# Kernel tuning notes

Measured on AMD Instinct MI355X. Metric: run time of the kernel, lower is better.

## Reference

```python
import jax, jax.numpy as jnp
import numpy as np

N_NODES = 100000
N_EDGES = 1600000
D_IN = 128
D_H = 128
N_LAYERS = 3
N_OUT = 10
N_GRAPHS = 64


def setup_inputs() -> dict:
    key = jax.random.key(0)
    ks = jax.random.split(key, 12)
    glorot = lambda k, fi, fo: jax.random.normal(k, (fi, fo), jnp.float32) * np.sqrt(2.0 / (fi + fo))
    return {
        "x": jax.random.normal(ks[0], (N_NODES, D_IN), jnp.float32),
        "edge_index": jax.random.randint(ks[1], (2, N_EDGES), 0, N_NODES, jnp.int64 if jax.config.jax_enable_x64 else jnp.int32),
        "batch": jnp.sort(jax.random.randint(ks[2], (N_NODES,), 0, N_GRAPHS)),
        "target_size": N_GRAPHS,
        "W1": glorot(ks[3], D_IN, D_H), "b1": jnp.zeros((D_H,), jnp.float32),
        "W2": glorot(ks[4], D_H, D_H), "b2": jnp.zeros((D_H,), jnp.float32),
        "W3": glorot(ks[5], D_H, D_H), "b3": jnp.zeros((D_H,), jnp.float32),
        "lin1_w": glorot(ks[6], N_LAYERS * D_H, D_H), "lin1_b": jnp.zeros((D_H,), jnp.float32),
        "lin2_w": glorot(ks[7], D_H, N_OUT), "lin2_b": jnp.zeros((N_OUT,), jnp.float32),
    }


def _gcn_conv(x, src, dst, norm, W, b, n_nodes):
    # PyG GCNConv: h = X W; out[dst] += norm * h[src]; out += b
    h = x @ W
    msg = h[src] * norm[:, None]            # [E+N, D_H] gathered messages
    out = jax.ops.segment_sum(msg, dst, num_segments=n_nodes)
    return out + b


def reference(x, edge_index, batch, target_size, W1, b1, W2, b2, W3, b3,
              lin1_w, lin1_b, lin2_w, lin2_b):
    n = x.shape[0]
    loops = jnp.arange(n, dtype=edge_index.dtype)
    src = jnp.concatenate([edge_index[0], loops])   # add self-loops (PyG default)
    dst = jnp.concatenate([edge_index[1], loops])
    deg = jax.ops.segment_sum(jnp.ones_like(src, dtype=x.dtype), dst, num_segments=n)
    dinv = jnp.where(deg > 0, jax.lax.rsqrt(deg), 0.0)
    norm = dinv[src] * dinv[dst]                    # symmetric normalization

    h1 = jax.nn.relu(_gcn_conv(x, src, dst, norm, W1, b1, n))
    h2 = jax.nn.relu(_gcn_conv(h1, src, dst, norm, W2, b2, n))
    h3 = jax.nn.relu(_gcn_conv(h2, src, dst, norm, W3, b3, n))
    h = jnp.concatenate([h1, h2, h3], axis=-1)      # JumpingKnowledge 'cat' -> [N, 3*D_H]

    # global_mean_pool over graphs
    counts = jax.ops.segment_sum(jnp.ones((n,), x.dtype), batch, num_segments=target_size)
    pooled = jax.ops.segment_sum(h, batch, num_segments=target_size)
    pooled = pooled / jnp.maximum(counts, 1.0)[:, None]

    g = jax.nn.relu(pooled @ lin1_w + lin1_b)       # dropout is identity at inference
    logits = g @ lin2_w + lin2_b
    return jax.nn.log_softmax(logits, axis=-1)
```

## Files before the change

### kernel.cpp

```cpp
#include <hip/hip_runtime.h>

#define NN 100000
#define NE 1600000
#define DH 128
#define NG 64

#define NBUCKU 98
#define EPB 4096
#define NBLK_BIN 391
#define CAP 20480

#define LDH 136
#define LDF 132

typedef __attribute__((ext_vector_type(2))) _Float16 half2v;
typedef __attribute__((ext_vector_type(4))) _Float16 half4;
typedef __attribute__((ext_vector_type(8))) _Float16 half8;
typedef __attribute__((ext_vector_type(4))) float f32x4;

__device__ inline unsigned int enc8(_Float16 h) {
  unsigned short b = __builtin_bit_cast(unsigned short, h);
  unsigned short r = (unsigned short)(b + 0x7F + ((b >> 8) & 1));
  return (unsigned int)(r >> 8);
}
__device__ inline half2v d02(unsigned int u) {
  return __builtin_bit_cast(half2v, (u << 8) & 0xFF00FF00u);
}
__device__ inline half2v d13(unsigned int u) {
  return __builtin_bit_cast(half2v, u & 0xFF00FF00u);
}

#define DEC4(u)                                                                         \
  acc[0] += d02(u.x); acc[1] += d13(u.x); acc[2] += d02(u.y); acc[3] += d13(u.y);       \
  acc[4] += d02(u.z); acc[5] += d13(u.z); acc[6] += d02(u.w); acc[7] += d13(u.w);

__device__ inline void gather_rows(const unsigned char* __restrict__ bp,
                                   const int* __restrict__ csr_src,
                                   int p, int e, half2v (&acc)[8]) {
  if (p + 3 < e) {
    int j0 = csr_src[p], j1 = csr_src[p + 1], j2 = csr_src[p + 2], j3 = csr_src[p + 3];
    uint4 c0 = *(const uint4*)(bp + (size_t)j0 * DH);
    uint4 c1 = *(const uint4*)(bp + (size_t)j1 * DH);
    uint4 c2 = *(const uint4*)(bp + (size_t)j2 * DH);
    uint4 c3 = *(const uint4*)(bp + (size_t)j3 * DH);
    p += 4;
    int pb = (p + 3 < e) ? p : p - 4;
    j0 = csr_src[pb]; j1 = csr_src[pb + 1]; j2 = csr_src[pb + 2]; j3 = csr_src[pb + 3];
    while (p + 3 < e) {
      uint4 n0 = *(const uint4*)(bp + (size_t)j0 * DH);
      uint4 n1 = *(const uint4*)(bp + (size_t)j1 * DH);
      uint4 n2 = *(const uint4*)(bp + (size_t)j2 * DH);
      uint4 n3 = *(const uint4*)(bp + (size_t)j3 * DH);
      p += 4;
      int pb2 = (p + 3 < e) ? p : p - 4;
      j0 = csr_src[pb2]; j1 = csr_src[pb2 + 1]; j2 = csr_src[pb2 + 2]; j3 = csr_src[pb2 + 3];
      DEC4(c0); DEC4(c1); DEC4(c2); DEC4(c3);
      c0 = n0; c1 = n1; c2 = n2; c3 = n3;
    }
    DEC4(c0); DEC4(c1); DEC4(c2); DEC4(c3);
  }
  for (; p < e; ++p) {
    uint4 u0 = *(const uint4*)(bp + (size_t)csr_src[p] * DH);
    DEC4(u0);
  }
}


__global__ __launch_bounds__(256) void k_pre(const float* __restrict__ W0,
                                             const float* __restrict__ W1,
                                             const float* __restrict__ W2,
                                             _Float16* __restrict__ Wt) {
  __shared__ _Float16 tile[128][LDH];
  int l = blockIdx.x, t = threadIdx.x;
  const float* W = (l == 0) ? W0 : (l == 1) ? W1 : W2;
#pragma unroll
  for (int i = 0; i < 64; ++i) {
    int idx = i * 256 + t;
    int r = idx >> 7, c = idx & 127;
    tile[c][r] = (_Float16)W[r * DH + c];
  }
  __syncthreads();
#pragma unroll
  for (int i = 0; i < 8; ++i) {
    int idx = i * 256 + t;
    int n = idx >> 4, c = (idx & 15) * 8;
    *(half8*)&Wt[(size_t)l * DH * DH + n * DH + c] = *(const half8*)&tile[n][c];
  }
}


__global__ __launch_bounds__(256) void k_build(const int* __restrict__ esrc,
                                               const int* __restrict__ edst,
                                               const int* __restrict__ batch,
                                               int* __restrict__ bucketCursor,
                                               unsigned int* __restrict__ pairs,
                                               int* __restrict__ startg) {
  int b = blockIdx.x, t = threadIdx.x;
  int gtid = b * 256 + t;

  if (gtid < NN) {
    int bat = batch[gtid];
    int prev = (gtid == 0) ? -1 : batch[gtid - 1];
    for (int g = prev + 1; g <= bat; ++g) startg[g] = gtid;
    if (gtid == NN - 1)
      for (int g = bat + 1; g <= NG; ++g) startg[g] = NN;
  }

  __shared__ int h[NBUCKU];
  __shared__ int cur[NBUCKU];
  if (t < NBUCKU) h[t] = 0;
  __syncthreads();
  int base = b * EPB;
  int dv[EPB / 256];
#pragma unroll
  for (int i = 0; i < EPB / 256; ++i) {
    int e = base + i * 256 + t;
    dv[i] = (e < NE) ? edst[e] : -1;
    if (e < NE) atomicAdd(&h[dv[i] >> 10], 1);
  }
  __syncthreads();
  if (t < NBUCKU) {
    int rel = atomicAdd(&bucketCursor[t], h[t]);
    cur[t] = t * CAP + rel;
  }
  __syncthreads();
#pragma unroll
  for (int i = 0; i < EPB / 256; ++i) {
    int e = base + i * 256 + t;
    if (e < NE) {
      int d = dv[i];
      int q = atomicAdd(&cur[d >> 10], 1);
      pairs[q] = ((unsigned int)esrc[e] << 10) | (unsigned int)(d & 1023);
    }
  }
}


__global__ __launch_bounds__(256) void k_finalize(const unsigned int* __restrict__ pairs,
                                                  const int* __restrict__ bucketCursor,
                                                  int* __restrict__ offA,
                                                  int* __restrict__ offB,
                                                  float* __restrict__ dinv,
                                                  int* __restrict__ csr_src) {
  __shared__ int cnt[1024];
  __shared__ int tsum[256];
  int b = blockIdx.x, t = threadIdx.x;
  int nodeBase = b << 10;
  for (int i = t; i < 1024; i += 256) cnt[i] = 0;
  __syncthreads();
  int pStart = b * CAP;
  int pEnd = pStart + bucketCursor[b];
  for (int p = pStart + t; p < pEnd; p += 256)
    atomicAdd(&cnt[pairs[p] & 1023], 1);
  __syncthreads();
  int c0 = cnt[t * 4], c1 = cnt[t * 4 + 1], c2 = cnt[t * 4 + 2], c3 = cnt[t * 4 + 3];
  tsum[t] = c0 + c1 + c2 + c3;
  __syncthreads();
  for (int off = 1; off < 256; off <<= 1) {
    int v = (t >= off) ? tsum[t - off] : 0;
    __syncthreads();
    tsum[t] += v;
    __syncthreads();
  }
  int basep = pStart + ((t > 0) ? tsum[t - 1] : 0);
  int e0 = basep, e1 = basep + c0, e2 = e1 + c1, e3 = e2 + c2;
  __syncthreads();
  cnt[t * 4] = e0; cnt[t * 4 + 1] = e1; cnt[t * 4 + 2] = e2; cnt[t * 4 + 3] = e3;
  int g = nodeBase + t * 4;
  if (g < NN)     { offA[g] = e0;     offB[g] = e1;      dinv[g] = rsqrtf((float)c0 + 1.f); }
  if (g + 1 < NN) { offA[g + 1] = e1; offB[g + 1] = e2;  dinv[g + 1] = rsqrtf((float)c1 + 1.f); }
  if (g + 2 < NN) { offA[g + 2] = e2; offB[g + 2] = e3;  dinv[g + 2] = rsqrtf((float)c2 + 1.f); }
  if (g + 3 < NN) { offA[g + 3] = e3; offB[g + 3] = e3 + c3; dinv[g + 3] = rsqrtf((float)c3 + 1.f); }
  __syncthreads();
  for (int p = pStart + t; p < pEnd; p += 256) {
    unsigned int pr = pairs[p];
    int pos = atomicAdd(&cnt[pr & 1023], 1);
    csr_src[pos] = (int)(pr >> 10);
  }
}


template <bool F32IN>
__global__ __launch_bounds__(256) void k_gemm(const void* __restrict__ Ap,
                                              const _Float16* __restrict__ Wt,
                                              const float* __restrict__ dinv,
                                              unsigned char* __restrict__ Out8) {
  __shared__ _Float16 Wl[128 * LDH];
  int tid = threadIdx.x;
  int rowBase = blockIdx.x * 128;

#pragma unroll
  for (int i = 0; i < 8; ++i) {
    int chunk = tid + i * 256;
    int r = chunk >> 4, c = (chunk & 15) * 8;
    *(half8*)&Wl[r * LDH + c] = *(const half8*)(Wt + r * DH + c);
  }

  int wv = tid >> 6;
  int lane = tid & 63;
  int n16 = lane & 15;
  int quad = lane >> 4;

  int r0 = rowBase + wv * 32 + n16;
  int r1 = r0 + 16;

  half8 af[2][4];
  if (F32IN) {
    const float* A = (const float*)Ap;
#pragma unroll
    for (int kk = 0; kk < 4; ++kk) {
      half8 z = {};
      if (r0 < NN) {
        float4 lo = *(const float4*)(A + (size_t)r0 * DH + quad * 8 + kk * 32);
        float4 hi = *(const float4*)(A + (size_t)r0 * DH + quad * 8 + kk * 32 + 4);
        z = (half8){(_Float16)lo.x, (_Float16)lo.y, (_Float16)lo.z, (_Float16)lo.w,
                    (_Float16)hi.x, (_Float16)hi.y, (_Float16)hi.z, (_Float16)hi.w};
      }
      af[0][kk] = z;
      half8 z1 = {};
      if (r1 < NN) {
        float4 lo = *(const float4*)(A + (size_t)r1 * DH + quad * 8 + kk * 32);
        float4 hi = *(const float4*)(A + (size_t)r1 * DH + quad * 8 + kk * 32 + 4);
        z1 = (half8){(_Float16)lo.x, (_Float16)lo.y, (_Float16)lo.z, (_Float16)lo.w,
                     (_Float16)hi.x, (_Float16)hi.y, (_Float16)hi.z, (_Float16)hi.w};
      }
      af[1][kk] = z1;
    }
  } else {
    const _Float16* A = (const _Float16*)Ap;
#pragma unroll
    for (int kk = 0; kk < 4; ++kk) {
      half8 z = {};
      if (r0 < NN) z = *(const half8*)(A + (size_t)r0 * DH + quad * 8 + kk * 32);
      af[0][kk] = z;
      half8 z1 = {};
      if (r1 < NN) z1 = *(const half8*)(A + (size_t)r1 * DH + quad * 8 + kk * 32);
      af[1][kk] = z1;
    }
  }
  __syncthreads();

  f32x4 acc[2][8];
#pragma unroll
  for (int mt = 0; mt < 2; ++mt)
#pragma unroll
    for (int ct = 0; ct < 8; ++ct) acc[mt][ct] = (f32x4){0.f, 0.f, 0.f, 0.f};

  const _Float16* bp = &Wl[n16 * LDH + quad * 8];
#pragma unroll
  for (int kk = 0; kk < 4; ++kk) {
#pragma unroll
    for (int ct = 0; ct < 8; ++ct) {
      half8 bf = *(const half8*)(bp + (size_t)ct * 16 * LDH + kk * 32);
      acc[0][ct] = __builtin_amdgcn_mfma_f32_16x16x32_f16(af[0][kk], bf, acc[0][ct], 0, 0, 0);
      acc[1][ct] = __builtin_amdgcn_mfma_f32_16x16x32_f16(af[1][kk], bf, acc[1][ct], 0, 0, 0);
    }
  }

  float dv[2][4];
#pragma unroll
  for (int mt = 0; mt < 2; ++mt)
#pragma unroll
    for (int r = 0; r < 4; ++r) {
      int gr = rowBase + wv * 32 + mt * 16 + quad * 4 + r;
      dv[mt][r] = (gr < NN) ? dinv[gr] : 0.f;
    }

  __syncthreads();
#pragma unroll
  for (int mt = 0; mt < 2; ++mt)
#pragma unroll
    for (int ct = 0; ct < 8; ++ct)
#pragma unroll
      for (int r = 0; r < 4; ++r)
        Wl[(wv * 32 + mt * 16 + quad * 4 + r) * LDH + ct * 16 + n16] =
            (_Float16)(acc[mt][ct][r] * dv[mt][r]);
  __syncthreads();

#pragma unroll
  for (int i = 0; i < 8; ++i) {
    int chunk = tid + i * 256;
    int r = chunk >> 4, c = (chunk & 15) * 8;
    int gr = rowBase + r;
    if (gr < NN) {
      half8 v = *(const half8*)&Wl[r * LDH + c];
      unsigned int lo = enc8(v[0]) | (enc8(v[1]) << 8) | (enc8(v[2]) << 16) | (enc8(v[3]) << 24);
      unsigned int hi = enc8(v[4]) | (enc8(v[5]) << 8) | (enc8(v[6]) << 16) | (enc8(v[7]) << 24);
      uint2 st = {lo, hi};
      *(uint2*)(Out8 + (size_t)gr * DH + c) = st;
    }
  }
}


__global__ __launch_bounds__(512) void k_fused(const unsigned char* __restrict__ hs8_in,
                                               const int* __restrict__ csr_src,
                                               const int* __restrict__ offA,
                                               const int* __restrict__ offB,
                                               const float* __restrict__ dinv,
                                               const float* __restrict__ bias,
                                               const int* __restrict__ batch,
                                               const int* __restrict__ startg,
                                               float* __restrict__ pooled,
                                               int colOff,
                                               const _Float16* __restrict__ Wt,
                                               unsigned char* __restrict__ hs8_out) {
  __shared__ _Float16 Hl[64 * LDH];
  __shared__ _Float16 Wl[128 * LDH];
  int tid = threadIdx.x;
  int n0 = blockIdx.x * 64;

#pragma unroll
  for (int i = 0; i < 4; ++i) {
    int chunk = tid + i * 512;
    int r = chunk >> 4, c = (chunk & 15) * 8;
    *(half8*)&Wl[r * LDH + c] = *(const half8*)(Wt + r * DH + c);
  }

  int nd = tid >> 3;
  int part = tid & 7;
  int n = n0 + nd;
  bool valid = (n < NN);

  half2v acc[8];
#pragma unroll
  for (int i = 0; i < 8; ++i) acc[i] = (half2v){(_Float16)0, (_Float16)0};

  if (valid) {
    const unsigned char* bp = hs8_in + part * 16;
    uint4 us = *(const uint4*)(bp + (size_t)n * DH);
    DEC4(us);
    gather_rows(bp, csr_src, offA[n], offB[n], acc);
  }

  float dv = valid ? dinv[n] : 0.f;
#pragma unroll
  for (int w = 0; w < 4; ++w) {
    int dim = part * 16 + w * 4;
    float4 b4 = *(const float4*)(bias + dim);
    float h0 = valid ? fmaxf(fmaf((float)acc[2 * w][0], dv, b4.x), 0.f) : 0.f;
    float h1 = valid ? fmaxf(fmaf((float)acc[2 * w + 1][0], dv, b4.y), 0.f) : 0.f;
    float h2 = valid ? fmaxf(fmaf((float)acc[2 * w][1], dv, b4.z), 0.f) : 0.f;
    float h3 = valid ? fmaxf(fmaf((float)acc[2 * w + 1][1], dv, b4.w), 0.f) : 0.f;
    half4 hh = {(_Float16)h0, (_Float16)h1, (_Float16)h2, (_Float16)h3};
    *(half4*)&Hl[nd * LDH + dim] = hh;
  }
  __syncthreads();

  if (tid < DH) {
    int nEnd = (n0 + 64 < NN) ? n0 + 64 : NN;
    int gF = batch[n0];
    int gL = batch[nEnd - 1];
    for (int g = gF; g <= gL; ++g) {
      int rs = (startg[g] > n0) ? startg[g] : n0;
      int re = (startg[g + 1] < nEnd) ? startg[g + 1] : nEnd;
      if (re > rs) {
        float sum = 0.f;
        for (int r2 = rs; r2 < re; ++r2) sum += (float)Hl[(r2 - n0) * LDH + tid];
        atomicAdd(&pooled[g * (3 * DH) + colOff + tid], sum);
      }
    }
  }

  int wv = tid >> 6;
  int lane = tid & 63;
  int n16 = lane & 15;
  int quad = lane >> 4;
  int m16 = wv >> 1;
  int ctB = (wv & 1) * 4;

  f32x4 acc2[4];
#pragma unroll
  for (int ct = 0; ct < 4; ++ct) acc2[ct] = (f32x4){0.f, 0.f, 0.f, 0.f};

  const _Float16* ap = &Hl[(m16 * 16 + n16) * LDH + quad * 8];
#pragma unroll
  for (int kk = 0; kk < 4; ++kk) {
    half8 af = *(const half8*)(ap + kk * 32);
#pragma unroll
    for (int ct = 0; ct < 4; ++ct) {
      half8 bf = *(const half8*)&Wl[((ctB + ct) * 16 + n16) * LDH + quad * 8 + kk * 32];
      acc2[ct] = __builtin_amdgcn_mfma_f32_16x16x32_f16(af, bf, acc2[ct], 0, 0, 0);
    }
  }

  float dvo[4];
#pragma unroll
  for (int rr = 0; rr < 4; ++rr) {
    int gr = n0 + m16 * 16 + quad * 4 + rr;
    dvo[rr] = (gr < NN) ? dinv[gr] : 0.f;
  }

  __syncthreads();
#pragma unroll
  for (int ct = 0; ct < 4; ++ct)
#pragma unroll
    for (int rr = 0; rr < 4; ++rr)
      Hl[(m16 * 16 + quad * 4 + rr) * LDH + (ctB + ct) * 16 + n16] =
          (_Float16)(acc2[ct][rr] * dvo[rr]);
  __syncthreads();

#pragma unroll
  for (int i = 0; i < 2; ++i) {
    int chunk = tid + i * 512;
    int r = chunk >> 4, c = (chunk & 15) * 8;
    int gr = n0 + r;
    if (gr < NN) {
      half8 v = *(const half8*)&Hl[r * LDH + c];
      unsigned int lo = enc8(v[0]) | (enc8(v[1]) << 8) | (enc8(v[2]) << 16) | (enc8(v[3]) << 24);
      unsigned int hi = enc8(v[4]) | (enc8(v[5]) << 8) | (enc8(v[6]) << 16) | (enc8(v[7]) << 24);
      uint2 st = {lo, hi};
      *(uint2*)(hs8_out + (size_t)gr * DH + c) = st;
    }
  }
}


__global__ __launch_bounds__(512) void k_aggregate(const unsigned char* __restrict__ hs8,
                                                   const int* __restrict__ csr_src,
                                                   const int* __restrict__ offA,
                                                   const int* __restrict__ offB,
                                                   const float* __restrict__ dinv,
                                                   const float* __restrict__ bias,
                                                   const int* __restrict__ batch,
                                                   const int* __restrict__ startg,
                                                   float* __restrict__ pooled,
                                                   int colOff) {
  __shared__ float stage[64][LDF];
  int tid = threadIdx.x;
  int n0 = blockIdx.x * 64;
  int nd = tid >> 3;
  int part = tid & 7;
  int n = n0 + nd;
  bool valid = (n < NN);

  half2v acc[8];
#pragma unroll
  for (int i = 0; i < 8; ++i) acc[i] = (half2v){(_Float16)0, (_Float16)0};

  if (valid) {
    const unsigned char* bp = hs8 + part * 16;
    uint4 us = *(const uint4*)(bp + (size_t)n * DH);
    DEC4(us);
    gather_rows(bp, csr_src, offA[n], offB[n], acc);
  }

  float dv = valid ? dinv[n] : 0.f;
#pragma unroll
  for (int w = 0; w < 4; ++w) {
    int dim = part * 16 + w * 4;
    float4 b4 = *(const float4*)(bias + dim);
    float4 r;
    r.x = valid ? fmaxf(fmaf((float)acc[2 * w][0], dv, b4.x), 0.f) : 0.f;
    r.y = valid ? fmaxf(fmaf((float)acc[2 * w + 1][0], dv, b4.y), 0.f) : 0.f;
    r.z = valid ? fmaxf(fmaf((float)acc[2 * w][1], dv, b4.z), 0.f) : 0.f;
    r.w = valid ? fmaxf(fmaf((float)acc[2 * w + 1][1], dv, b4.w), 0.f) : 0.f;
    *(float4*)&stage[nd][dim] = r;
  }
  __syncthreads();

  if (tid < DH) {
    int nEnd = (n0 + 64 < NN) ? n0 + 64 : NN;
    int gF = batch[n0];
    int gL = batch[nEnd - 1];
    for (int g = gF; g <= gL; ++g) {
      int rs = (startg[g] > n0) ? startg[g] : n0;
      int re = (startg[g + 1] < nEnd) ? startg[g + 1] : nEnd;
      if (re > rs) {
        float sum = 0.f;
        for (int r2 = rs; r2 < re; ++r2) sum += stage[r2 - n0][tid];
        atomicAdd(&pooled[g * (3 * DH) + colOff + tid], sum);
      }
    }
  }
}


__global__ __launch_bounds__(128) void k_head(const float* __restrict__ pooled,
                                              const int* __restrict__ startg,
                                              const float* __restrict__ l1w,
                                              const float* __restrict__ l1b,
                                              const float* __restrict__ l2w,
                                              const float* __restrict__ l2b,
                                              float* __restrict__ out) {
  __shared__ float pr[3 * DH];
  __shared__ float grow[DH];
  __shared__ float lg[16];
  int g = blockIdx.x, t = threadIdx.x;
  float cnt = (float)(startg[g + 1] - startg[g]);
  float inv = 1.0f / fmaxf(cnt, 1.0f);
  for (int k = t; k < 3 * DH; k += 128) pr[k] = pooled[g * (3 * DH) + k] * inv;
  __syncthreads();
  float acc = l1b[t];
  for (int k = 0; k < 3 * DH; ++k) acc = fmaf(pr[k], l1w[k * DH + t], acc);
  grow[t] = fmaxf(acc, 0.f);
  __syncthreads();
  if (t < 10) {
    float a = l2b[t];
    for (int k = 0; k < DH; ++k) a = fmaf(grow[k], l2w[k * 10 + t], a);
    lg[t] = a;
  }
  __syncthreads();
  if (t < 10) {
    float m = lg[0];
    for (int i = 1; i < 10; ++i) m = fmaxf(m, lg[i]);
    float sum = 0.f;
    for (int i = 0; i < 10; ++i) sum += expf(lg[i] - m);
    out[g * 10 + t] = lg[t] - m - logf(sum);
  }
}


extern "C" void kernel_launch(void* const* d_in, const int* in_sizes, int n_in,
                              void* d_out, int out_size, void* d_ws, size_t ws_size,
                              hipStream_t stream) {
  const float* x = (const float*)d_in[0];
  const int* ei = (const int*)d_in[1];
  const int* esrc = ei;
  const int* edst = ei + NE;
  const int* batch = (const int*)d_in[2];
  const float* W0 = (const float*)d_in[4];
  const float* W1 = (const float*)d_in[6];
  const float* W2 = (const float*)d_in[8];
  const float* B[3] = {(const float*)d_in[5], (const float*)d_in[7], (const float*)d_in[9]};
  const float* l1w = (const float*)d_in[10];
  const float* l1b = (const float*)d_in[11];
  const float* l2w = (const float*)d_in[12];
  const float* l2b = (const float*)d_in[13];
  float* out = (float*)d_out;

  char* ws = (char*)d_ws;
  size_t off = 0;
  auto alloc = [&](size_t bytes) {
    char* p = ws + off;
    off = (off + bytes + 255) & ~(size_t)255;
    return p;
  };
  float* pooled = (float*)alloc((size_t)NG * 3 * DH * 4);
  int* bucketCursor = (int*)alloc(NBUCKU * 4);
  size_t msBytes = (size_t)NG * 3 * DH * 4 + 512;

  int* offA = (int*)alloc((size_t)NN * 4);
  int* offB = (int*)alloc((size_t)NN * 4);
  float* dinv = (float*)alloc((size_t)NN * 4);
  int* startg = (int*)alloc((NG + 1) * 4);
  _Float16* Wt = (_Float16*)alloc((size_t)3 * DH * DH * 2);
  unsigned char* hs8A = (unsigned char*)alloc((size_t)NN * DH);
  unsigned char* hs8B = (unsigned char*)alloc((size_t)NN * DH);
  unsigned int* pairs = (unsigned int*)alloc((size_t)NBUCKU * CAP * 4);
  int* csr_src = (int*)alloc((size_t)NBUCKU * CAP * 4);

  hipMemsetAsync(pooled, 0, msBytes, stream);

  k_pre<<<3, 256, 0, stream>>>(W0, W1, W2, Wt);
  k_build<<<NBLK_BIN, 256, 0, stream>>>(esrc, edst, batch, bucketCursor, pairs, startg);
  k_finalize<<<NBUCKU, 256, 0, stream>>>(pairs, bucketCursor, offA, offB, dinv, csr_src);

  k_gemm<true><<<(NN + 127) / 128, 256, 0, stream>>>((const void*)x, Wt, dinv, hs8A);

  int nFusedBlk = (NN + 63) / 64;
  k_fused<<<nFusedBlk, 512, 0, stream>>>(hs8A, csr_src, offA, offB, dinv, B[0], batch,
                                         startg, pooled, 0,
                                         Wt + (size_t)1 * DH * DH, hs8B);
  k_fused<<<nFusedBlk, 512, 0, stream>>>(hs8B, csr_src, offA, offB, dinv, B[1], batch,
                                         startg, pooled, DH,
                                         Wt + (size_t)2 * DH * DH, hs8A);

  k_aggregate<<<nFusedBlk, 512, 0, stream>>>(hs8A, csr_src, offA, offB, dinv, B[2],
                                             batch, startg, pooled, 2 * DH);

  k_head<<<NG, 128, 0, stream>>>(pooled, startg, l1w, l1b, l2w, l2b, out);
}
```

Measured before the change: 342.0 us.

## Use finer 256-node CSR buckets and fold weight transpose into build kernel

Buckets now cover 256 destination nodes instead of 1024, so the finalize kernel runs 391 blocks instead of 98 and each thread handles one node, with a smaller per-bucket capacity. The weight transpose/convert kernel is merged into the edge-binning kernel, where the first three blocks also write the transposed fp16 weights. This removes one launch and spreads the CSR build across more blocks. The cost is more global bucket atomics and more shared-memory use in k_build, plus a tighter 5120-entry capacity per bucket that could overflow on skewed degree distributions.

```diff
diff --git a/kernel.cpp b/kernel.cpp
--- a/kernel.cpp
+++ b/kernel.cpp
@@ -5,10 +5,10 @@
 #define DH 128
 #define NG 64
 
-#define NBUCKU 98
+#define NBUCK 391
 #define EPB 4096
 #define NBLK_BIN 391
-#define CAP 20480
+#define CAP 5120
 
 #define LDH 136
 #define LDF 132
@@ -66,37 +66,38 @@
 }
 
 
-__global__ __launch_bounds__(256) void k_pre(const float* __restrict__ W0,
-                                             const float* __restrict__ W1,
-                                             const float* __restrict__ W2,
-                                             _Float16* __restrict__ Wt) {
-  __shared__ _Float16 tile[128][LDH];
-  int l = blockIdx.x, t = threadIdx.x;
-  const float* W = (l == 0) ? W0 : (l == 1) ? W1 : W2;
-#pragma unroll
-  for (int i = 0; i < 64; ++i) {
-    int idx = i * 256 + t;
-    int r = idx >> 7, c = idx & 127;
-    tile[c][r] = (_Float16)W[r * DH + c];
-  }
-  __syncthreads();
-#pragma unroll
-  for (int i = 0; i < 8; ++i) {
-    int idx = i * 256 + t;
-    int n = idx >> 4, c = (idx & 15) * 8;
-    *(half8*)&Wt[(size_t)l * DH * DH + n * DH + c] = *(const half8*)&tile[n][c];
-  }
-}
-
-
 __global__ __launch_bounds__(256) void k_build(const int* __restrict__ esrc,
                                                const int* __restrict__ edst,
                                                const int* __restrict__ batch,
+                                               const float* __restrict__ W0,
+                                               const float* __restrict__ W1,
+                                               const float* __restrict__ W2,
                                                int* __restrict__ bucketCursor,
                                                unsigned int* __restrict__ pairs,
-                                               int* __restrict__ startg) {
+                                               int* __restrict__ startg,
+                                               _Float16* __restrict__ Wt) {
+  __shared__ _Float16 tile[128][LDH];
+  __shared__ int h[NBUCK];
+  __shared__ int cur[NBUCK];
   int b = blockIdx.x, t = threadIdx.x;
   int gtid = b * 256 + t;
+
+  if (b < 3) {
+    const float* W = (b == 0) ? W0 : (b == 1) ? W1 : W2;
+#pragma unroll
+    for (int i = 0; i < 64; ++i) {
+      int idx = i * 256 + t;
+      int r = idx >> 7, c = idx & 127;
+      tile[c][r] = (_Float16)W[r * DH + c];
+    }
+    __syncthreads();
+#pragma unroll
+    for (int i = 0; i < 8; ++i) {
+      int idx = i * 256 + t;
+      int n = idx >> 4, c = (idx & 15) * 8;
+      *(half8*)&Wt[(size_t)b * DH * DH + n * DH + c] = *(const half8*)&tile[n][c];
+    }
+  }
 
   if (gtid < NN) {
     int bat = batch[gtid];
@@ -106,9 +107,7 @@
       for (int g = bat + 1; g <= NG; ++g) startg[g] = NN;
   }
 
-  __shared__ int h[NBUCKU];
-  __shared__ int cur[NBUCKU];
-  if (t < NBUCKU) h[t] = 0;
+  for (int i = t; i < NBUCK; i += 256) h[i] = 0;
   __syncthreads();
   int base = b * EPB;
   int dv[EPB / 256];
@@ -116,12 +115,12 @@
   for (int i = 0; i < EPB / 256; ++i) {
     int e = base + i * 256 + t;
     dv[i] = (e < NE) ? edst[e] : -1;
-    if (e < NE) atomicAdd(&h[dv[i] >> 10], 1);
-  }
-  __syncthreads();
-  if (t < NBUCKU) {
-    int rel = atomicAdd(&bucketCursor[t], h[t]);
-    cur[t] = t * CAP + rel;
+    if (e < NE) atomicAdd(&h[dv[i] >> 8], 1);
+  }
+  __syncthreads();
+  for (int i = t; i < NBUCK; i += 256) {
+    int rel = atomicAdd(&bucketCursor[i], h[i]);
+    cur[i] = i * CAP + rel;
   }
   __syncthreads();
 #pragma unroll
@@ -129,8 +128,8 @@
     int e = base + i * 256 + t;
     if (e < NE) {
       int d = dv[i];
-      int q = atomicAdd(&cur[d >> 10], 1);
-      pairs[q] = ((unsigned int)esrc[e] << 10) | (unsigned int)(d & 1023);
+      int q = atomicAdd(&cur[d >> 8], 1);
+      pairs[q] = ((unsigned int)esrc[e] << 8) | (unsigned int)(d & 255);
     }
   }
 }
@@ -142,19 +141,19 @@
                                                   int* __restrict__ offB,
                                                   float* __restrict__ dinv,
                                                   int* __restrict__ csr_src) {
-  __shared__ int cnt[1024];
+  __shared__ int cnt[256];
   __shared__ int tsum[256];
   int b = blockIdx.x, t = threadIdx.x;
-  int nodeBase = b << 10;
-  for (int i = t; i < 1024; i += 256) cnt[i] = 0;
+  int g = (b << 8) + t;
+  cnt[t] = 0;
   __syncthreads();
   int pStart = b * CAP;
   int pEnd = pStart + bucketCursor[b];
   for (int p = pStart + t; p < pEnd; p += 256)
-    atomicAdd(&cnt[pairs[p] & 1023], 1);
-  __syncthreads();
-  int c0 = cnt[t * 4], c1 = cnt[t * 4 + 1], c2 = cnt[t * 4 + 2], c3 = cnt[t * 4 + 3];
-  tsum[t] = c0 + c1 + c2 + c3;
+    atomicAdd(&cnt[pairs[p] & 255], 1);
+  __syncthreads();
+  int c = cnt[t];
+  tsum[t] = c;
   __syncthreads();
   for (int off = 1; off < 256; off <<= 1) {
     int v = (t >= off) ? tsum[t - off] : 0;
@@ -163,19 +162,17 @@
     __syncthreads();
   }
   int basep = pStart + ((t > 0) ? tsum[t - 1] : 0);
-  int e0 = basep, e1 = basep + c0, e2 = e1 + c1, e3 = e2 + c2;
-  __syncthreads();
-  cnt[t * 4] = e0; cnt[t * 4 + 1] = e1; cnt[t * 4 + 2] = e2; cnt[t * 4 + 3] = e3;
-  int g = nodeBase + t * 4;
-  if (g < NN)     { offA[g] = e0;     offB[g] = e1;      dinv[g] = rsqrtf((float)c0 + 1.f); }
-  if (g + 1 < NN) { offA[g + 1] = e1; offB[g + 1] = e2;  dinv[g + 1] = rsqrtf((float)c1 + 1.f); }
-  if (g + 2 < NN) { offA[g + 2] = e2; offB[g + 2] = e3;  dinv[g + 2] = rsqrtf((float)c2 + 1.f); }
-  if (g + 3 < NN) { offA[g + 3] = e3; offB[g + 3] = e3 + c3; dinv[g + 3] = rsqrtf((float)c3 + 1.f); }
+  if (g < NN) {
+    offA[g] = basep;
+    offB[g] = basep + c;
+    dinv[g] = rsqrtf((float)c + 1.f);
+  }
+  cnt[t] = basep;
   __syncthreads();
   for (int p = pStart + t; p < pEnd; p += 256) {
     unsigned int pr = pairs[p];
-    int pos = atomicAdd(&cnt[pr & 1023], 1);
-    csr_src[pos] = (int)(pr >> 10);
+    int pos = atomicAdd(&cnt[pr & 255], 1);
+    csr_src[pos] = (int)(pr >> 8);
   }
 }
 
@@ -537,8 +534,8 @@
     return p;
   };
   float* pooled = (float*)alloc((size_t)NG * 3 * DH * 4);
-  int* bucketCursor = (int*)alloc(NBUCKU * 4);
-  size_t msBytes = (size_t)NG * 3 * DH * 4 + 512;
+  int* bucketCursor = (int*)alloc(NBUCK * 4);
+  size_t msBytes = ((size_t)NG * 3 * DH * 4 + NBUCK * 4 + 255) & ~(size_t)255;
 
   int* offA = (int*)alloc((size_t)NN * 4);
   int* offB = (int*)alloc((size_t)NN * 4);
@@ -547,14 +544,14 @@
   _Float16* Wt = (_Float16*)alloc((size_t)3 * DH * DH * 2);
   unsigned char* hs8A = (unsigned char*)alloc((size_t)NN * DH);
   unsigned char* hs8B = (unsigned char*)alloc((size_t)NN * DH);
-  unsigned int* pairs = (unsigned int*)alloc((size_t)NBUCKU * CAP * 4);
-  int* csr_src = (int*)alloc((size_t)NBUCKU * CAP * 4);
+  unsigned int* pairs = (unsigned int*)alloc((size_t)NBUCK * CAP * 4);
+  int* csr_src = (int*)alloc((size_t)NBUCK * CAP * 4);
 
   hipMemsetAsync(pooled, 0, msBytes, stream);
 
-  k_pre<<<3, 256, 0, stream>>>(W0, W1, W2, Wt);
-  k_build<<<NBLK_BIN, 256, 0, stream>>>(esrc, edst, batch, bucketCursor, pairs, startg);
-  k_finalize<<<NBUCKU, 256, 0, stream>>>(pairs, bucketCursor, offA, offB, dinv, csr_src);
+  k_build<<<NBLK_BIN, 256, 0, stream>>>(esrc, edst, batch, W0, W1, W2,
+                                        bucketCursor, pairs, startg, Wt);
+  k_finalize<<<NBUCK, 256, 0, stream>>>(pairs, bucketCursor, offA, offB, dinv, csr_src);
 
   k_gemm<true><<<(NN + 127) / 128, 256, 0, stream>>>((const void*)x, Wt, dinv, hs8A);
 
```

Measured after the change: 314.3 us (median of 2 runs). 8.1% less time.
